# Performance work log

Hardware: AMD Instinct MI355X
Metric: run time of the kernel (lower is better)

The kernel has to match this reference:

```python
import jax, jax.numpy as jnp
import numpy as np

H = 256
NUM_REL = 460
NUM_ENT = 20000
B = 4096
CUR_TS = 10
PATH_LEN = 8


def _gru_step(x, h, W_ih, W_hh, b_ih, b_hh):
    # PyTorch GRUCell math
    gi = x @ W_ih.T + b_ih          # [B, 3H]
    gh = h @ W_hh.T + b_hh          # [B, 3H]
    ir, iz, inn = jnp.split(gi, 3, axis=1)
    hr, hz, hn = jnp.split(gh, 3, axis=1)
    r = jax.nn.sigmoid(ir + hr)
    z = jax.nn.sigmoid(iz + hz)
    n = jnp.tanh(inn + r * hn)
    return (1.0 - z) * n + z * h


def setup_inputs() -> dict:
    key = jax.random.key(0)
    ks = jax.random.split(key, 24)
    s = 1.0 / np.sqrt(H)
    f32 = jnp.float32
    d = {
        "pre_emb": jax.random.normal(ks[0], (NUM_ENT, H), f32),
        "r_emb": jax.random.normal(ks[1], (NUM_REL, H), f32),
        "partial_embeding": jax.random.normal(ks[2], (B, CUR_TS * NUM_REL), f32),
        # params (uniform-ish linear init scaled by 1/sqrt(H))
        "W_map1": jax.random.normal(ks[3], (2 * H, H), f32) * s,
        "b_map1": jax.random.normal(ks[4], (2 * H,), f32) * s,
        "W_map2": jax.random.normal(ks[5], (H, 2 * H), f32) * s,
        "b_map2": jax.random.normal(ks[6], (H,), f32) * s,
        "W_h1": jax.random.normal(ks[7], (H, H), f32) * s,
        "b_h1": jax.random.normal(ks[8], (H,), f32) * s,
        "W_h2": jax.random.normal(ks[9], (H, H), f32) * s,
        "b_h2": jax.random.normal(ks[10], (H,), f32) * s,
        "W_attn": jax.random.normal(ks[11], (H, H), f32) * s,
        "b_attn": jax.random.normal(ks[12], (H,), f32) * s,
        "W_align": jax.random.normal(ks[13], (H, H), f32) * s,
        "b_align": jax.random.normal(ks[14], (H,), f32) * s,
        "W_ih": jax.random.normal(ks[15], (3 * H, H), f32) * s,
        "W_hh": jax.random.normal(ks[16], (3 * H, H), f32) * s,
        "b_ih": jax.random.normal(ks[17], (3 * H,), f32) * s,
        "b_hh": jax.random.normal(ks[18], (3 * H,), f32) * s,
        "all_triples": jax.random.randint(ks[19], (B, 3), 0, NUM_REL, dtype=jnp.int64)
        if jax.config.jax_enable_x64 else jax.random.randint(ks[19], (B, 3), 0, NUM_REL, dtype=jnp.int32),
        "cur_ts": CUR_TS,
        "num_rel": NUM_REL,
    }
    return d


def reference(pre_emb, r_emb, partial_embeding,
              W_map1, b_map1, W_map2, b_map2,
              W_h1, b_h1, W_h2, b_h2,
              W_attn, b_attn, W_align, b_align,
              W_ih, W_hh, b_ih, b_hh,
              all_triples, cur_ts, num_rel):
    # rel_mapping1 -> rel_mapping2
    mapped_rel = (r_emb @ W_map1.T + b_map1) @ W_map2.T + b_map2     # [R, H]
    q_rel = mapped_rel[all_triples[:, 1]]                            # [B, H]

    # attention logits base (constant over timesteps): linear_attn(q_rel) @ mapped_rel.T
    attn_base = (q_rel @ W_attn.T + b_attn) @ mapped_rel.T           # [B, R]

    start_ts = max(cur_ts - PATH_LEN, 0)
    nb = partial_embeding.shape[0]
    cur_seq = partial_embeding.reshape(nb, cur_ts, num_rel)[:, start_ts:cur_ts]  # [B, T, R]
    cur_seq = jnp.swapaxes(cur_seq, 0, 1)                            # [T, B, R]

    h0 = jnp.zeros((nb, H), dtype=pre_emb.dtype)

    def step(h, cur):
        attn = cur * attn_base
        attn = jnp.where(attn == 0, jnp.asarray(-1e9, attn.dtype), attn)
        attn = jax.nn.softmax(attn, axis=1)
        x = attn @ mapped_rel                                        # [B, H]
        return _gru_step(x, h, W_ih, W_hh, b_ih, b_hh), None

    gru_hidden, _ = jax.lax.scan(step, h0, cur_seq)

    # predicted history embedding + match loss (MSE)
    predicted_hist = 0.1 * ((q_rel @ W_h1.T + b_h1) @ W_h2.T + b_h2) + q_rel
    match_loss = jnp.mean((predicted_hist - gru_hidden) ** 2)

    # forward_forth, distmult scoring
    h2 = _gru_step(q_rel, predicted_hist, W_ih, W_hh, b_ih, b_hh)    # [B, H]
    aligned_all = pre_emb @ W_align.T + b_align                      # [E, H]
    sub = aligned_all[all_triples[:, 0]]                             # [B, H]
    score_logits = (sub * h2) @ aligned_all.T                        # [B, E]
    score = jax.nn.sigmoid(score_logits)

    # BCE(sigmoid(logits), one_hot(obj)) in stable logits form without
    # materializing the dense one-hot label matrix:
    # mean over B*E of [ softplus(x) - x * label ]
    obj = all_triples[:, 2]
    pos_logits = score_logits[jnp.arange(nb), obj]
    path_loss = (jnp.sum(jax.nn.softplus(score_logits)) - jnp.sum(pos_logits)) / (nb * score_logits.shape[1])

    return match_loss, path_loss, score
```

## Files before the change

kernel.cpp:

```cpp
#include <hip/hip_runtime.h>
#include <hip/hip_bf16.h>

typedef __hip_bfloat16 bf16;
typedef __attribute__((ext_vector_type(8))) short short8;
typedef __attribute__((ext_vector_type(4))) float f32x4;
typedef __attribute__((ext_vector_type(4))) short short4v;

#define NREL 460
#define KP   480
#define NENT 20000
#define NENT_PAD 20096
#define NB   4096

__device__ inline float sigmoidf_(float x){ return 1.f/(1.f+__expf(-x)); }

__device__ inline void gload16(const bf16* g, bf16* l){
  __builtin_amdgcn_global_load_lds(
      (const __attribute__((address_space(1))) unsigned int*)g,
      (__attribute__((address_space(3))) unsigned int*)l, 16, 0, 0);
}

__device__ __forceinline__ void fgemm_body(
    const float* __restrict__ A, int lda, int arows,
    const float* __restrict__ B, int ldb,
    const float* __restrict__ bias,
    float* __restrict__ C, int ldc, int K, int mode,
    const float* __restrict__ add_src, bf16* __restrict__ ct_out,
    int bx, int by)
{
  __shared__ __align__(16) float As[32][68];
  __shared__ __align__(16) float Bs[32][68];
  const int tid = threadIdx.x;
  const int row0 = bx*64, col0 = by*64;
  const int tx = tid & 15, ty = tid >> 4;
  float acc[4][4] = {};
  for (int k0 = 0; k0 < K; k0 += 32){
    __syncthreads();
    #pragma unroll
    for (int s = 0; s < 2; ++s){
      int slot = tid + s*256;
      int r = slot >> 3, c4 = (slot & 7)*4;
      int ra = row0 + r; if (ra >= arows) ra = arows - 1;
      float4 v = *(const float4*)(A + (long)ra*lda + k0 + c4);
      As[c4+0][r] = v.x; As[c4+1][r] = v.y; As[c4+2][r] = v.z; As[c4+3][r] = v.w;
      float4 w = *(const float4*)(B + (long)(col0 + r)*ldb + k0 + c4);
      Bs[c4+0][r] = w.x; Bs[c4+1][r] = w.y; Bs[c4+2][r] = w.z; Bs[c4+3][r] = w.w;
    }
    __syncthreads();
    #pragma unroll
    for (int kk = 0; kk < 32; ++kk){
      float4 a4 = *(const float4*)(&As[kk][ty*4]);
      float4 b4 = *(const float4*)(&Bs[kk][tx*4]);
      float av[4] = {a4.x, a4.y, a4.z, a4.w};
      float bv[4] = {b4.x, b4.y, b4.z, b4.w};
      #pragma unroll
      for (int i = 0; i < 4; ++i)
        #pragma unroll
        for (int j = 0; j < 4; ++j) acc[i][j] += av[i]*bv[j];
    }
  }
  const int rb = row0 + ty*4, cb = col0 + tx*4;
  if (mode == 1){
    #pragma unroll
    for (int i = 0; i < 4; ++i){
      float4 v = {acc[i][0], acc[i][1], acc[i][2], acc[i][3]};
      *(float4*)(C + (long)(rb+i)*ldc + cb) = v;
      int rr = rb + i;
      if (rr < KP){
        #pragma unroll
        for (int j = 0; j < 4; ++j)
          ct_out[(cb+j)*KP + rr] = __float2bfloat16(rr < NREL ? acc[i][j] : 0.f);
      }
    }
  } else if (mode == 2){
    #pragma unroll
    for (int i = 0; i < 4; ++i){
      float4 v;
      #pragma unroll
      for (int j = 0; j < 4; ++j)
        ((float*)&v)[j] = 0.1f*(acc[i][j] + bias[cb+j]) + add_src[(long)(rb+i)*ldc + cb+j];
      *(float4*)(C + (long)(rb+i)*ldc + cb) = v;
    }
  } else {
    float bv[4] = {0,0,0,0};
    if (bias){ bv[0]=bias[cb]; bv[1]=bias[cb+1]; bv[2]=bias[cb+2]; bv[3]=bias[cb+3]; }
    #pragma unroll
    for (int i = 0; i < 4; ++i){
      float4 v = {acc[i][0]+bv[0], acc[i][1]+bv[1], acc[i][2]+bv[2], acc[i][3]+bv[3]};
      *(float4*)(C + (long)(rb+i)*ldc + cb) = v;
    }
  }
}

__global__ __launch_bounds__(256) void k_fgemm(
    const float* A, int lda, int arows, const float* B, int ldb,
    const float* bias, float* C, int ldc, int K, int mode,
    const float* add_src, bf16* ct_out){
  fgemm_body(A, lda, arows, B, ldb, bias, C, ldc, K, mode, add_src, ct_out,
             blockIdx.x, blockIdx.y);
}

struct FDesc {
  const float* A; const float* B; const float* bias; float* C;
  const float* add; bf16* ct;
  int lda, ldb, ldc, K, arows, mode;
};

__global__ __launch_bounds__(256) void k_fgemm_multi(FDesc d0, FDesc d1, FDesc d2,
                                                     int y1, int y2){
  int y = blockIdx.y;
  FDesc d; int by;
  if (y < y1){ d = d0; by = y; }
  else if (y < y2){ d = d1; by = y - y1; }
  else { d = d2; by = y - y2; }
  fgemm_body(d.A, d.lda, d.arows, d.B, d.ldb, d.bias, d.C, d.ldc, d.K, d.mode,
             d.add, d.ct, blockIdx.x, by);
}

__global__ __launch_bounds__(256) void k_h2(const float* __restrict__ M_ih,
    const float* __restrict__ b_ih, const float* __restrict__ ghp,
    const float* __restrict__ ph, float* __restrict__ h2_rel){
  int r = blockIdx.x, c = threadIdx.x;
  float rg = sigmoidf_(M_ih[r*768+c]       + b_ih[c]       + ghp[r*768+c]);
  float zg = sigmoidf_(M_ih[r*768+256+c]   + b_ih[256+c]   + ghp[r*768+256+c]);
  float ng = tanhf    (M_ih[r*768+512+c]   + b_ih[512+c]   + rg*ghp[r*768+512+c]);
  h2_rel[r*256+c] = (1.f - zg)*ng + zg*ph[r*256+c];
}

__global__ void k_f2bf3(const float4* __restrict__ s0, short4v* __restrict__ d0, int n0,
                        const float4* __restrict__ s1, short4v* __restrict__ d1, int n1,
                        const float4* __restrict__ s2, short4v* __restrict__ d2, int n2,
                        short4v* __restrict__ pad0, int n3, double* __restrict__ dz){
  int i = blockIdx.x*256 + threadIdx.x;
  if (i < n0+n1+n2){
    const float4* s; short4v* d; int j;
    if (i < n0){ s = s0; d = d0; j = i; }
    else if (i < n0+n1){ s = s1; d = d1; j = i-n0; }
    else { s = s2; d = d2; j = i-n0-n1; }
    float4 v = s[j];
    bf16 a = __float2bfloat16(v.x), b = __float2bfloat16(v.y);
    bf16 c = __float2bfloat16(v.z), e = __float2bfloat16(v.w);
    short4v o; o.x = *(short*)&a; o.y = *(short*)&b; o.z = *(short*)&c; o.w = *(short*)&e;
    d[j] = o;
  } else if (i < n0+n1+n2+n3){
    short4v z = {0,0,0,0};
    pad0[i - (n0+n1+n2)] = z;
  } else if (i < n0+n1+n2+n3+4){
    dz[i - (n0+n1+n2+n3)] = 0.0;
  }
}

__global__ __launch_bounds__(256) void k_soft_makep(const float* __restrict__ partial,
    const float* __restrict__ attn_base, const int* __restrict__ trips,
    bf16* __restrict__ attn_all,
    const bf16* __restrict__ Qbf, const float* __restrict__ h2_rel,
    bf16* __restrict__ P){
  int bid = blockIdx.x;
  if (bid >= NB/4){
    int i = (bid - NB/4)*256 + threadIdx.x;
    int b = i >> 8, k = i & 255;
    int s = trips[b*3+0], rel = trips[b*3+1];
    P[i] = __float2bfloat16(__bfloat162float(Qbf[s*256+k]) * h2_rel[rel*256+k]);
    return;
  }
  int wave = threadIdx.x >> 6, lane = threadIdx.x & 63;
  int b = bid*4 + wave;
  int rel = trips[b*3+1];
  const float* base = attn_base + (long)rel*512;
  float bs[8];
  #pragma unroll
  for (int s = 0; s < 8; ++s){
    int idx = s*64 + lane;
    bs[s] = (idx < NREL) ? base[idx] : 0.f;
  }
  const float* cur0 = partial + (long)b*4600 + 2*NREL;
  for (int t = 0; t < 8; ++t){
    const float* cur = cur0 + t*NREL;
    float v[8]; float mx = -1e30f;
    #pragma unroll
    for (int s = 0; s < 8; ++s){
      int idx = s*64 + lane;
      float val = -1e30f;
      if (idx < NREL){
        float pz = cur[idx]*bs[s];
        val = (pz == 0.f) ? -1e9f : pz;
      }
      v[s] = val; mx = fmaxf(mx, val);
    }
    #pragma unroll
    for (int off = 32; off >= 1; off >>= 1) mx = fmaxf(mx, __shfl_xor(mx, off));
    float sum = 0.f;
    #pragma unroll
    for (int s = 0; s < 8; ++s){
      int idx = s*64 + lane;
      if (idx < NREL){ v[s] = __expf(v[s]-mx); sum += v[s]; }
    }
    #pragma unroll
    for (int off = 32; off >= 1; off >>= 1) sum += __shfl_xor(sum, off);
    float inv = 1.f/sum;
    long obase = ((long)t*NB + b)*KP;
    #pragma unroll
    for (int s = 0; s < 8; ++s){
      int idx = s*64 + lane;
      if (idx < KP) attn_all[obase + idx] = __float2bfloat16(idx < NREL ? v[s]*inv : 0.f);
    }
  }
}

template<int MODE>
__global__ __launch_bounds__(256) void k_gemm128(
    const bf16* __restrict__ A, int lda,
    const bf16* __restrict__ B, int ldb,
    const float* __restrict__ bias,
    void* __restrict__ C, long ldc,
    int K, int n_valid, double* __restrict__ sp_sum,
    const int* __restrict__ trips)
{
  __shared__ __align__(16) bf16 sbuf[16384];
  __shared__ float wsum[8];
  const int tid = threadIdx.x;
  const int lane = tid & 63, wave = tid >> 6;
  const long row0 = (long)blockIdx.x * 128;
  const long col0 = (long)blockIdx.y * 128;
  const int sr = tid >> 2;
  const int sc = (tid & 3) * 8;
  const bf16* Ag0 = A + (row0 + sr)*lda + sc;
  const bf16* Ag1 = A + (row0 + 64 + sr)*lda + sc;
  const bf16* Bg0 = B + (col0 + sr)*ldb + sc;
  const bf16* Bg1 = B + (col0 + 64 + sr)*ldb + sc;
  const int wr = (wave >> 1)*64, wc = (wave & 1)*64;
  const int rA = lane & 15, kA = (lane >> 4)*8;
  f32x4 acc[4][4] = {};
  const int nt = K >> 5;
  bf16* As_ = sbuf;
  bf16* Bs_ = sbuf + 8192;
  gload16(Ag0, As_ + tid*8);
  gload16(Ag1, As_ + 2048 + tid*8);
  gload16(Bg0, Bs_ + tid*8);
  gload16(Bg1, Bs_ + 2048 + tid*8);
  int cur = 0;
  for (int t = 0; t < nt; ++t){
    if (t + 1 < nt){
      const int k0 = (t+1) << 5;
      const int nxt = cur ^ 1;
      gload16(Ag0 + k0, As_ + nxt*4096 + tid*8);
      gload16(Ag1 + k0, As_ + nxt*4096 + 2048 + tid*8);
      gload16(Bg0 + k0, Bs_ + nxt*4096 + tid*8);
      gload16(Bg1 + k0, Bs_ + nxt*4096 + 2048 + tid*8);
      asm volatile("s_waitcnt vmcnt(4)" ::: "memory");
    } else {
      asm volatile("s_waitcnt vmcnt(0)" ::: "memory");
    }
    __builtin_amdgcn_s_barrier();
    short8 a[4], b[4];
    #pragma unroll
    for (int m = 0; m < 4; ++m) a[m] = *(const short8*)(As_ + cur*4096 + (wr + m*16 + rA)*32 + kA);
    #pragma unroll
    for (int n = 0; n < 4; ++n) b[n] = *(const short8*)(Bs_ + cur*4096 + (wc + n*16 + rA)*32 + kA);
    asm volatile("s_waitcnt lgkmcnt(0)" ::: "memory");
    __builtin_amdgcn_s_barrier();
    #pragma unroll
    for (int m = 0; m < 4; ++m)
      #pragma unroll
      for (int n = 0; n < 4; ++n)
        acc[m][n] = __builtin_amdgcn_mfma_f32_16x16x32_bf16(a[m], b[n], acc[m][n], 0,0,0);
    cur ^= 1;
  }
  const int ri = (lane >> 4)*4, ci = lane & 15;
  __syncthreads();
  if constexpr (MODE == 1){
    bf16* epi = sbuf + wave*1152;
    const int rrow = lane >> 2, q = lane & 3;
    #pragma unroll
    for (int m = 0; m < 4; ++m){
      #pragma unroll
      for (int n = 0; n < 4; ++n){
        long c = col0 + wc + n*16 + ci;
        float bv = bias ? bias[c] : 0.f;
        #pragma unroll
        for (int i = 0; i < 4; ++i)
          epi[(ri+i)*72 + n*16 + ci] = __float2bfloat16(acc[m][n][i] + bv);
      }
      long gr = row0 + wr + m*16 + rrow;
      bf16* gp = (bf16*)C + gr*ldc + col0 + wc + q*16;
      const bf16* lp = epi + rrow*72 + q*16;
      *(short8*)(gp)     = *(const short8*)(lp);
      *(short8*)(gp + 8) = *(const short8*)(lp + 8);
    }
  } else {
    float* epi = (float*)sbuf + wave*1088;
    const int rrow = lane >> 2, q = lane & 3;
    const bool maybe = (col0 + wc) < 464;
    float spart = 0.f, ppart = 0.f;
    #pragma unroll
    for (int m = 0; m < 4; ++m){
      int obj[4];
      if (maybe){
        #pragma unroll
        for (int i = 0; i < 4; ++i)
          obj[i] = trips[3*(int)(row0 + wr + m*16 + ri + i) + 2];
      }
      #pragma unroll
      for (int n = 0; n < 4; ++n){
        long c = col0 + wc + n*16 + ci;
        bool cv = (c < n_valid);
        #pragma unroll
        for (int i = 0; i < 4; ++i){
          float v = acc[m][n][i];
          float sg = 0.f;
          if (cv){
            float e = __expf(-fabsf(v));
            float tt = 1.f + e;
            float rr = __builtin_amdgcn_rcpf(tt);
            sg = (v >= 0.f) ? rr : 1.f - rr;
            spart += fmaxf(v, 0.f) + e*(0.9404f - 0.2537f*e);
            if (maybe && c == obj[i]) ppart += v;
          }
          epi[(ri+i)*68 + n*16 + ci + 2] = sg;
        }
      }
      long gr = row0 + wr + m*16 + rrow;
      long c16 = col0 + wc + q*16;
      if (c16 < n_valid){
        float* gp = (float*)C + gr*ldc + c16;
        const float* lp = epi + rrow*68 + q*16 + 2;
        *(float2*)(gp)      = *(const float2*)(lp);
        *(float4*)(gp + 2)  = *(const float4*)(lp + 2);
        *(float4*)(gp + 6)  = *(const float4*)(lp + 6);
        *(float4*)(gp + 10) = *(const float4*)(lp + 10);
        *(float2*)(gp + 14) = *(const float2*)(lp + 14);
      }
    }
    #pragma unroll
    for (int off = 32; off >= 1; off >>= 1){
      spart += __shfl_xor(spart, off);
      ppart += __shfl_xor(ppart, off);
    }
    if (lane == 0){ wsum[wave] = spart; wsum[4+wave] = ppart; }
    __syncthreads();
    if (tid == 0)
      atomicAdd(sp_sum, (double)(wsum[0]+wsum[1]+wsum[2]+wsum[3]));
    if (tid == 1)
      atomicAdd(sp_sum+1, (double)(wsum[4]+wsum[5]+wsum[6]+wsum[7]));
  }
}

__global__ __launch_bounds__(512) void k_scan(
    const bf16* __restrict__ gi_all,
    const bf16* __restrict__ W_hh_bf,
    const float* __restrict__ b_hh,
    const float* __restrict__ ph,
    const int* __restrict__ trips,
    double* __restrict__ dsum)
{
  __shared__ __align__(16) bf16 hl[16*264];
  __shared__ __align__(16) bf16 gbuf[2][16*768];
  __shared__ float red[8];
  const int tid = threadIdx.x;
  const int lane = tid & 63, wave = tid >> 6;
  const int brow0 = blockIdx.x * 16;
  const int rA = lane & 15, kA = (lane >> 4) * 8;
  const int ci = lane & 15, rbase = (lane >> 4) * 4;
  float hreg[2][4] = {};
  float bh[3][2];
  #pragma unroll
  for (int f = 0; f < 2; ++f){
    int cf = wave*32 + f*16 + ci;
    bh[0][f] = b_hh[cf]; bh[1][f] = b_hh[256+cf]; bh[2][f] = b_hh[512+cf];
  }
  short8 warr[3][2][6];
  #pragma unroll
  for (int g = 0; g < 3; ++g)
    #pragma unroll
    for (int f = 0; f < 2; ++f)
      #pragma unroll
      for (int k = 0; k < 6; ++k)
        warr[g][f][k] = *(const short8*)(W_hh_bf + (g*256 + wave*32 + f*16 + rA)*256 + k*32 + kA);
  {
    const bf16* src = gi_all + (long)brow0 * 768;
    #pragma unroll
    for (int i = 0; i < 3; ++i){
      int off = (wave*3 + i)*512 + lane*8;
      gload16(src + off, gbuf[0] + off);
    }
  }
  int cur = 0;
  for (int t = 0; t < 8; ++t){
    f32x4 acc[3][2] = {};
    if (t > 0){
      #pragma unroll
      for (int k = 0; k < 8; ++k){
        short8 a = *(const short8*)(hl + rA*264 + k*32 + kA);
        #pragma unroll
        for (int g = 0; g < 3; ++g)
          #pragma unroll
          for (int f = 0; f < 2; ++f){
            short8 b;
            if (k < 6) b = warr[g][f][k];
            else b = *(const short8*)(W_hh_bf + (g*256 + wave*32 + f*16 + rA)*256 + k*32 + kA);
            acc[g][f] = __builtin_amdgcn_mfma_f32_16x16x32_bf16(a, b, acc[g][f], 0,0,0);
          }
      }
    }
    asm volatile("s_waitcnt lgkmcnt(0) vmcnt(0)" ::: "memory");
    __builtin_amdgcn_s_barrier();
    if (t < 7){
      const bf16* src = gi_all + ((long)(t+1)*NB + brow0) * 768;
      bf16* dst = gbuf[cur ^ 1];
      #pragma unroll
      for (int i = 0; i < 3; ++i){
        int off = (wave*3 + i)*512 + lane*8;
        gload16(src + off, dst + off);
      }
    }
    const bf16* gl = gbuf[cur];
    #pragma unroll
    for (int f = 0; f < 2; ++f){
      int cf = wave*32 + f*16 + ci;
      #pragma unroll
      for (int i = 0; i < 4; ++i){
        int rloc = rbase + i;
        float gir = __bfloat162float(gl[rloc*768 + cf]);
        float giz = __bfloat162float(gl[rloc*768 + 256 + cf]);
        float gin = __bfloat162float(gl[rloc*768 + 512 + cf]);
        float rg = sigmoidf_(gir + acc[0][f][i] + bh[0][f]);
        float zg = sigmoidf_(giz + acc[1][f][i] + bh[1][f]);
        float ng = tanhf(gin + rg*(acc[2][f][i] + bh[2][f]));
        float hn = (1.f - zg)*ng + zg*hreg[f][i];
        hreg[f][i] = hn;
        hl[rloc*264 + cf] = __float2bfloat16(hn);
      }
    }
    asm volatile("s_waitcnt lgkmcnt(0)" ::: "memory");
    __builtin_amdgcn_s_barrier();
    cur ^= 1;
  }
  float d = 0.f;
  #pragma unroll
  for (int f = 0; f < 2; ++f){
    int cf = wave*32 + f*16 + ci;
    #pragma unroll
    for (int i = 0; i < 4; ++i){
      int rel = trips[(brow0 + rbase + i)*3 + 1];
      float diff = ph[rel*256 + cf] - hreg[f][i];
      d += diff*diff;
    }
  }
  #pragma unroll
  for (int off = 32; off >= 1; off >>= 1) d += __shfl_xor(d, off);
  if (lane == 0) red[wave] = d;
  __syncthreads();
  if (tid == 0){
    float s = 0.f;
    #pragma unroll
    for (int w = 0; w < 8; ++w) s += red[w];
    atomicAdd(dsum, (double)s);
  }
}

__global__ void k_final(const double* __restrict__ d, float* __restrict__ out){
  out[0] = (float)(d[0] / (4096.0*256.0));
  out[1] = (float)((d[1] - d[2]) / (4096.0*20000.0));
}

extern "C" void kernel_launch(void* const* d_in, const int* in_sizes, int n_in,
                              void* d_out, int out_size, void* d_ws, size_t ws_size,
                              hipStream_t stream){
  const float* pre_emb = (const float*)d_in[0];
  const float* r_emb   = (const float*)d_in[1];
  const float* partial = (const float*)d_in[2];
  const float* W_map1  = (const float*)d_in[3];
  const float* b_map1  = (const float*)d_in[4];
  const float* W_map2  = (const float*)d_in[5];
  const float* b_map2  = (const float*)d_in[6];
  const float* W_h1    = (const float*)d_in[7];
  const float* b_h1    = (const float*)d_in[8];
  const float* W_h2    = (const float*)d_in[9];
  const float* b_h2    = (const float*)d_in[10];
  const float* W_attn  = (const float*)d_in[11];
  const float* b_attn  = (const float*)d_in[12];
  const float* W_align = (const float*)d_in[13];
  const float* b_align = (const float*)d_in[14];
  const float* W_ih    = (const float*)d_in[15];
  const float* W_hh    = (const float*)d_in[16];
  const float* b_ih    = (const float*)d_in[17];
  const float* b_hh    = (const float*)d_in[18];
  const int*   trips   = (const int*)d_in[19];
  float* out = (float*)d_out;

  char* w = (char*)d_ws;
  auto alloc = [&](size_t bytes)->char*{
    char* r = w; w += (bytes + 255) & ~size_t(255); return r;
  };
  double* dsum      = (double*)alloc(128);
  float* t1         = (float*)alloc(512*512*4);
  float* mapped     = (float*)alloc(512*256*4);
  float* a1         = (float*)alloc(512*256*4);
  float* th         = (float*)alloc(512*256*4);
  float* ph         = (float*)alloc(512*256*4);
  float* M_ih       = (float*)alloc(512*768*4);
  float* ghp        = (float*)alloc(512*768*4);
  float* attn_base  = (float*)alloc(512*512*4);
  float* h2_rel     = (float*)alloc(NREL*256*4);
  bf16*  M_ihT      = (bf16*)alloc(768*KP*2);
  bf16*  W_hh_bf    = (bf16*)alloc(768*256*2);
  bf16*  W_align_bf = (bf16*)alloc(256*256*2);
  bf16*  Q_bf       = (bf16*)alloc((size_t)NENT_PAD*256*2);
  bf16*  P_bf       = (bf16*)alloc((size_t)NB*256*2);
  bf16*  attn_all   = (bf16*)alloc((size_t)8*NB*KP*2);
  bf16*  gi_all     = (bf16*)alloc((size_t)8*NB*768*2);
  bf16*  pre_bf     = attn_all;

  {
    int n0 = NENT*256/4, n1 = 768*256/4, n2 = 256*256/4;
    int n3 = (NENT_PAD-NENT)*256/4;
    int ntot = n0+n1+n2+n3+4;
    k_f2bf3<<<(ntot+255)/256, 256, 0, stream>>>(
        (const float4*)pre_emb, (short4v*)pre_bf, n0,
        (const float4*)W_hh, (short4v*)W_hh_bf, n1,
        (const float4*)W_align, (short4v*)W_align_bf, n2,
        (short4v*)(pre_bf + (size_t)NENT*256), n3, dsum);
  }

  k_fgemm<<<dim3(8,8),256,0,stream>>>(r_emb,256,NREL, W_map1,256, b_map1, t1,512, 256, 0, nullptr, nullptr);
  k_fgemm<<<dim3(8,4),256,0,stream>>>(t1,512,512, W_map2,512, b_map2, mapped,256, 512, 0, nullptr, nullptr);
  {
    FDesc d0 = { mapped, W_ih,   nullptr, M_ih, nullptr, M_ihT, 256, 256, 768, 256, 512, 1 };
    FDesc d1 = { mapped, W_attn, b_attn,  a1,   nullptr, nullptr, 256, 256, 256, 256, 512, 0 };
    FDesc d2 = { mapped, W_h1,   b_h1,    th,   nullptr, nullptr, 256, 256, 256, 256, 512, 0 };
    k_fgemm_multi<<<dim3(8,20),256,0,stream>>>(d0, d1, d2, 12, 16);
  }
  k_fgemm<<<dim3(8,4),256,0,stream>>>(th,256,512, W_h2,256, b_h2, ph,256, 256, 2, mapped, nullptr);
  {
    FDesc d0 = { a1, mapped, nullptr, attn_base, nullptr, nullptr, 256, 256, 512, 256, 512, 0 };
    FDesc d1 = { ph, W_hh,   b_hh,    ghp,       nullptr, nullptr, 256, 256, 768, 256, 512, 0 };
    k_fgemm_multi<<<dim3(8,20),256,0,stream>>>(d0, d1, d1, 8, 20);
  }
  k_h2<<<NREL,256,0,stream>>>(M_ih, b_ih, ghp, ph, h2_rel);

  {
    dim3 g(NENT_PAD/128, 256/128);
    k_gemm128<1><<<g,256,0,stream>>>(pre_bf, 256, W_align_bf, 256, b_align,
                                     Q_bf, 256, 256, 0, nullptr, nullptr);
  }
  k_soft_makep<<<NB/4 + NB,256,0,stream>>>(partial, attn_base, trips, attn_all,
                                           Q_bf, h2_rel, P_bf);

  {
    dim3 g(8*NB/128, 768/128);
    k_gemm128<1><<<g,256,0,stream>>>(attn_all, KP, M_ihT, KP, b_ih,
                                     gi_all, 768, KP, 0, nullptr, nullptr);
  }

  k_scan<<<NB/16,512,0,stream>>>(gi_all, W_hh_bf, b_hh, ph, trips, dsum);

  {
    dim3 g(NB/128, NENT_PAD/128);
    k_gemm128<2><<<g,256,0,stream>>>(P_bf, 256, Q_bf, 256, nullptr,
                                     out+2, NENT, 256, NENT, dsum+1, trips);
  }
  k_final<<<1,1,0,stream>>>(dsum, out);
}
```

Measured before the change: 397.9 us.

## Enlarge bf16 GEMM tile to 256x128 with two A sub-tiles per wave

The shared bf16 MFMA GEMM kernel now computes a 256-row by 128-column tile per block, with each wave holding two 64x64 accumulator sets. Each B fragment is reused across twice as many MFMAs, which cuts LDS and global traffic per flop. Grids are halved along the row dimension and NENT_PAD is raised so the entity count divides by 256. In exchange, accumulator register pressure doubles (launch bounds request two blocks per CU), LDS use grows, and fewer blocks run on the smaller GEMMs, which may leave CUs idle.

```diff
diff --git a/kernel.cpp b/kernel.cpp
--- a/kernel.cpp
+++ b/kernel.cpp
@@ -9,7 +9,7 @@
 #define NREL 460
 #define KP   480
 #define NENT 20000
-#define NENT_PAD 20096
+#define NENT_PAD 20224
 #define NB   4096
 
 __device__ inline float sigmoidf_(float x){ return 1.f/(1.f+__expf(-x)); }
@@ -208,7 +208,7 @@
 }
 
 template<int MODE>
-__global__ __launch_bounds__(256) void k_gemm128(
+__global__ __launch_bounds__(256, 2) void k_gemm128(
     const bf16* __restrict__ A, int lda,
     const bf16* __restrict__ B, int ldb,
     const float* __restrict__ bias,
@@ -216,54 +216,63 @@
     int K, int n_valid, double* __restrict__ sp_sum,
     const int* __restrict__ trips)
 {
-  __shared__ __align__(16) bf16 sbuf[16384];
+  __shared__ __align__(16) bf16 sbuf[24576];
   __shared__ float wsum[8];
   const int tid = threadIdx.x;
   const int lane = tid & 63, wave = tid >> 6;
-  const long row0 = (long)blockIdx.x * 128;
+  const long row0 = (long)blockIdx.x * 256;
   const long col0 = (long)blockIdx.y * 128;
   const int sr = tid >> 2;
   const int sc = (tid & 3) * 8;
   const bf16* Ag0 = A + (row0 + sr)*lda + sc;
   const bf16* Ag1 = A + (row0 + 64 + sr)*lda + sc;
+  const bf16* Ag2 = A + (row0 + 128 + sr)*lda + sc;
+  const bf16* Ag3 = A + (row0 + 192 + sr)*lda + sc;
   const bf16* Bg0 = B + (col0 + sr)*ldb + sc;
   const bf16* Bg1 = B + (col0 + 64 + sr)*ldb + sc;
+  bf16* As_ = sbuf;
+  bf16* Bs_ = sbuf + 16384;
   const int wr = (wave >> 1)*64, wc = (wave & 1)*64;
   const int rA = lane & 15, kA = (lane >> 4)*8;
-  f32x4 acc[4][4] = {};
+  f32x4 acc[2][4][4] = {};
   const int nt = K >> 5;
-  bf16* As_ = sbuf;
-  bf16* Bs_ = sbuf + 8192;
-  gload16(Ag0, As_ + tid*8);
-  gload16(Ag1, As_ + 2048 + tid*8);
-  gload16(Bg0, Bs_ + tid*8);
-  gload16(Bg1, Bs_ + 2048 + tid*8);
+  auto stage = [&](int t, int buf){
+    const int k0 = t << 5;
+    gload16(Ag0 + k0, As_ + buf*8192 + tid*8);
+    gload16(Ag1 + k0, As_ + buf*8192 + 2048 + tid*8);
+    gload16(Ag2 + k0, As_ + buf*8192 + 4096 + tid*8);
+    gload16(Ag3 + k0, As_ + buf*8192 + 6144 + tid*8);
+    gload16(Bg0 + k0, Bs_ + buf*4096 + tid*8);
+    gload16(Bg1 + k0, Bs_ + buf*4096 + 2048 + tid*8);
+  };
+  stage(0, 0);
   int cur = 0;
   for (int t = 0; t < nt; ++t){
     if (t + 1 < nt){
-      const int k0 = (t+1) << 5;
-      const int nxt = cur ^ 1;
-      gload16(Ag0 + k0, As_ + nxt*4096 + tid*8);
-      gload16(Ag1 + k0, As_ + nxt*4096 + 2048 + tid*8);
-      gload16(Bg0 + k0, Bs_ + nxt*4096 + tid*8);
-      gload16(Bg1 + k0, Bs_ + nxt*4096 + 2048 + tid*8);
-      asm volatile("s_waitcnt vmcnt(4)" ::: "memory");
+      stage(t + 1, cur ^ 1);
+      asm volatile("s_waitcnt vmcnt(6)" ::: "memory");
     } else {
       asm volatile("s_waitcnt vmcnt(0)" ::: "memory");
     }
     __builtin_amdgcn_s_barrier();
-    short8 a[4], b[4];
-    #pragma unroll
-    for (int m = 0; m < 4; ++m) a[m] = *(const short8*)(As_ + cur*4096 + (wr + m*16 + rA)*32 + kA);
-    #pragma unroll
-    for (int n = 0; n < 4; ++n) b[n] = *(const short8*)(Bs_ + cur*4096 + (wc + n*16 + rA)*32 + kA);
+    short8 a[2][4], b[4];
+    #pragma unroll
+    for (int at = 0; at < 2; ++at)
+      #pragma unroll
+      for (int m = 0; m < 4; ++m)
+        a[at][m] = *(const short8*)(As_ + cur*8192 + (at*128 + wr + m*16 + rA)*32 + kA);
+    #pragma unroll
+    for (int n = 0; n < 4; ++n)
+      b[n] = *(const short8*)(Bs_ + cur*4096 + (wc + n*16 + rA)*32 + kA);
     asm volatile("s_waitcnt lgkmcnt(0)" ::: "memory");
     __builtin_amdgcn_s_barrier();
     #pragma unroll
-    for (int m = 0; m < 4; ++m)
-      #pragma unroll
-      for (int n = 0; n < 4; ++n)
-        acc[m][n] = __builtin_amdgcn_mfma_f32_16x16x32_bf16(a[m], b[n], acc[m][n], 0,0,0);
+    for (int at = 0; at < 2; ++at)
+      #pragma unroll
+      for (int m = 0; m < 4; ++m)
+        #pragma unroll
+        for (int n = 0; n < 4; ++n)
+          acc[at][m][n] = __builtin_amdgcn_mfma_f32_16x16x32_bf16(a[at][m], b[n], acc[at][m][n], 0,0,0);
     cur ^= 1;
   }
   const int ri = (lane >> 4)*4, ci = lane & 15;
@@ -272,6 +281,8 @@
     bf16* epi = sbuf + wave*1152;
     const int rrow = lane >> 2, q = lane & 3;
     #pragma unroll
+    for (int at = 0; at < 2; ++at)
+    #pragma unroll
     for (int m = 0; m < 4; ++m){
       #pragma unroll
       for (int n = 0; n < 4; ++n){
@@ -279,9 +290,9 @@
         float bv = bias ? bias[c] : 0.f;
         #pragma unroll
         for (int i = 0; i < 4; ++i)
-          epi[(ri+i)*72 + n*16 + ci] = __float2bfloat16(acc[m][n][i] + bv);
-      }
-      long gr = row0 + wr + m*16 + rrow;
+          epi[(ri+i)*72 + n*16 + ci] = __float2bfloat16(acc[at][m][n][i] + bv);
+      }
+      long gr = row0 + at*128 + wr + m*16 + rrow;
       bf16* gp = (bf16*)C + gr*ldc + col0 + wc + q*16;
       const bf16* lp = epi + rrow*72 + q*16;
       *(short8*)(gp)     = *(const short8*)(lp);
@@ -293,12 +304,14 @@
     const bool maybe = (col0 + wc) < 464;
     float spart = 0.f, ppart = 0.f;
     #pragma unroll
+    for (int at = 0; at < 2; ++at)
+    #pragma unroll
     for (int m = 0; m < 4; ++m){
       int obj[4];
       if (maybe){
         #pragma unroll
         for (int i = 0; i < 4; ++i)
-          obj[i] = trips[3*(int)(row0 + wr + m*16 + ri + i) + 2];
+          obj[i] = trips[3*(int)(row0 + at*128 + wr + m*16 + ri + i) + 2];
       }
       #pragma unroll
       for (int n = 0; n < 4; ++n){
@@ -306,7 +319,7 @@
         bool cv = (c < n_valid);
         #pragma unroll
         for (int i = 0; i < 4; ++i){
-          float v = acc[m][n][i];
+          float v = acc[at][m][n][i];
           float sg = 0.f;
           if (cv){
             float e = __expf(-fabsf(v));
@@ -319,7 +332,7 @@
           epi[(ri+i)*68 + n*16 + ci + 2] = sg;
         }
       }
-      long gr = row0 + wr + m*16 + rrow;
+      long gr = row0 + at*128 + wr + m*16 + rrow;
       long c16 = col0 + wc + q*16;
       if (c16 < n_valid){
         float* gp = (float*)C + gr*ldc + c16;
@@ -539,7 +552,7 @@
   k_h2<<<NREL,256,0,stream>>>(M_ih, b_ih, ghp, ph, h2_rel);
 
   {
-    dim3 g(NENT_PAD/128, 256/128);
+    dim3 g(NENT_PAD/256, 256/128);
     k_gemm128<1><<<g,256,0,stream>>>(pre_bf, 256, W_align_bf, 256, b_align,
                                      Q_bf, 256, 256, 0, nullptr, nullptr);
   }
@@ -547,7 +560,7 @@
                                            Q_bf, h2_rel, P_bf);
 
   {
-    dim3 g(8*NB/128, 768/128);
+    dim3 g(8*NB/256, 768/128);
     k_gemm128<1><<<g,256,0,stream>>>(attn_all, KP, M_ihT, KP, b_ih,
                                      gi_all, 768, KP, 0, nullptr, nullptr);
   }
@@ -555,7 +568,7 @@
   k_scan<<<NB/16,512,0,stream>>>(gi_all, W_hh_bf, b_hh, ph, trips, dsum);
 
   {
-    dim3 g(NB/128, NENT_PAD/128);
+    dim3 g(NB/256, NENT_PAD/128);
     k_gemm128<2><<<g,256,0,stream>>>(P_bf, 256, Q_bf, 256, nullptr,
                                      out+2, NENT, 256, NENT, dsum+1, trips);
   }
```

New measurement: 399.1 us. No clear change (+0.3%).
